# Performance work log

Measured on AMD Instinct MI355X. Metric: run time of the kernel, lower is better.

Reference implementation:

```python
import jax, jax.numpy as jnp
import numpy as np
from jax import lax

STRENGTH = 1.0
NORMALIZE = True


def setup_inputs() -> dict:
    key = jax.random.key(0)
    k1, k2 = jax.random.split(key)
    hidden_states = jax.random.normal(k1, (8, 4096, 1024), dtype=jnp.float32)
    # probe_weight is [k, hidden]; Q = orth(probe_weight.T) -> [hidden, k] orthonormal columns
    pw = jax.random.normal(k2, (1024, 16), dtype=jnp.float32)
    Q, _ = jnp.linalg.qr(pw)  # [hidden, k], orthonormal columns
    return {"hidden_states": hidden_states, "Q": Q}


def reference(hidden_states, Q):
    if NORMALIZE:
        old_norms = jnp.linalg.norm(hidden_states, axis=2, keepdims=True)  # [B,S,1]
    # Sequential Gram-Schmidt removal per direction (column of Q), as in the torch loop.
    def step(h, q):  # h: [B,S,H], q: [H]
        coef = jnp.einsum('bsh,h->bs', h, q)          # projection coefficient
        h = h - STRENGTH * coef[..., None] * q        # subtract component along q
        return h, None
    h, _ = lax.scan(step, hidden_states, Q.T)          # scan over k directions
    if NORMALIZE:
        norms = jnp.linalg.norm(h, axis=2, keepdims=True)
        h = h / norms * old_norms
    return h
```

## Files before the change

kernel.cpp:

```cpp
#include <hip/hip_runtime.h>
#include <hip/hip_bf16.h>

constexpr int HID = 1024;
constexpr int KD  = 16;
constexpr int TM  = 16;
constexpr int NW  = 8;
constexpr int TPB = 8;

typedef short bf16x8 __attribute__((ext_vector_type(8)));
typedef float f32x4  __attribute__((ext_vector_type(4)));

__device__ __forceinline__ short f2b(float x) {
    __hip_bfloat16 b = __float2bfloat16(x);
    return *reinterpret_cast<short*>(&b);
}
__device__ __forceinline__ float b2f(short s) {
    return __uint_as_float(((unsigned int)(unsigned short)s) << 16);
}

__global__ void q_setup(const float* __restrict__ Qf,
                        short* __restrict__ Qt, short* __restrict__ Qa) {
    const int idx = blockIdx.x*256 + threadIdx.x;
    if (idx < 16*HID) {
        const int r = idx >> 10, k = idx & 1023;
        Qt[idx] = f2b(Qf[k*KD + r]);
        const int gs = idx >> 4, dir = idx & 15;
        const int jslot = gs >> 4, rr = gs & 15;
        const int w = jslot >> 3, jl = jslot & 7;
        const int p = jl >> 1, odd = jl & 1;
        const int col = w*128 + p*32 + (rr >> 2)*8 + odd*4 + (rr & 3);
        Qa[idx] = f2b(Qf[col*KD + dir]);
    }
}

#define SCHED_FENCE() __builtin_amdgcn_sched_barrier(0)

__device__ __forceinline__ void stage_tile(float* ldsBuf, const float* Hbase,
                                           int w, int lane) {
    #pragma unroll
    for (int i = 0; i < 8; ++i) {
        const int rr = w*2 + (i >> 2);
        const int qq = i & 3;
        const int s  = qq*64 + lane;
        const float* g = Hbase + rr*1024 + ((s ^ (rr & 7)) << 2);
        const float* l = ldsBuf + rr*1024 + qq*256;
        __builtin_amdgcn_global_load_lds(
            (const __attribute__((address_space(1))) void*)g,
            (__attribute__((address_space(3))) void*)l, 16, 0, 0);
    }
}

__global__ __launch_bounds__(NW*64)
void probe_removal_dma8(const float* __restrict__ H,
                        const short* __restrict__ Qt,
                        const short* __restrict__ Qa,
                        float* __restrict__ out)
{
    const int lane = threadIdx.x & 63;
    const int w    = threadIdx.x >> 6;
    const int r    = lane & 15;
    const int q    = lane >> 4;

    __shared__ __align__(16) float Hb[2][TM][HID];
    __shared__ __align__(16) float ctr[NW][TM][20];
    __shared__ float s2p[NW][TM];

    const int tile0 = blockIdx.x * TPB;

    bf16x8 bq[4];
    #pragma unroll
    for (int kt = 0; kt < 4; ++kt)
        bq[kt] = *reinterpret_cast<const bf16x8*>(Qt + r*1024 + w*128 + q*8 + kt*32);
    bf16x8 aq0[4], aq1[4];
    #pragma unroll
    for (int p = 0; p < 4; ++p) {
        if (q < 2) {
            aq0[p] = *reinterpret_cast<const bf16x8*>(Qa + ((w*8 + 2*p    )*16 + r)*KD + q*8);
            aq1[p] = *reinterpret_cast<const bf16x8*>(Qa + ((w*8 + 2*p + 1)*16 + r)*KD + q*8);
        } else {
            #pragma unroll
            for (int i = 0; i < 8; ++i) { aq0[p][i] = 0; aq1[p][i] = 0; }
        }
    }
    SCHED_FENCE();

    stage_tile(&Hb[0][0][0], H + (size_t)tile0*TM*HID, w, lane);
    SCHED_FENCE();
    stage_tile(&Hb[1][0][0], H + (size_t)(tile0+1)*TM*HID, w, lane);
    SCHED_FENCE();
    asm volatile("s_waitcnt vmcnt(8)" ::: "memory");
    SCHED_FENCE();
    __builtin_amdgcn_s_barrier();

    #pragma unroll
    for (int t = 0; t < TPB; ++t) {
        const int cur = t & 1;
        const char* HbC = (const char*)&Hb[cur][0][0];

        bf16x8 af[4];
        f32x4 acc0 = {0.f,0.f,0.f,0.f}, acc1 = {0.f,0.f,0.f,0.f};
        float s2 = 0.f;
        #pragma unroll
        for (int kt = 0; kt < 4; ++kt) {
            const int P  = w*32 + kt*8 + q*2;
            const int sx = P ^ (r & 7);
            const float4 x = *(const float4*)(HbC + r*4096 + sx*16);
            const float4 y = *(const float4*)(HbC + r*4096 + (sx^1)*16);
            s2 = fmaf(x.x,x.x, fmaf(x.y,x.y, fmaf(x.z,x.z, fmaf(x.w,x.w, s2))));
            s2 = fmaf(y.x,y.x, fmaf(y.y,y.y, fmaf(y.z,y.z, fmaf(y.w,y.w, s2))));
            bf16x8 a;
            a[0]=f2b(x.x); a[1]=f2b(x.y); a[2]=f2b(x.z); a[3]=f2b(x.w);
            a[4]=f2b(y.x); a[5]=f2b(y.y); a[6]=f2b(y.z); a[7]=f2b(y.w);
            af[kt] = a;
            if (kt & 1) acc1 = __builtin_amdgcn_mfma_f32_16x16x32_bf16(a, bq[kt], acc1, 0, 0, 0);
            else        acc0 = __builtin_amdgcn_mfma_f32_16x16x32_bf16(a, bq[kt], acc0, 0, 0, 0);
        }
        const f32x4 acc = acc0 + acc1;
        s2 += __shfl_xor(s2, 16);
        s2 += __shfl_xor(s2, 32);

        #pragma unroll
        for (int i = 0; i < 4; ++i) ctr[w][q*4 + i][r] = acc[i];
        if (q == 0) s2p[w][r] = s2;

        asm volatile("s_waitcnt lgkmcnt(0)" ::: "memory");
        SCHED_FENCE();
        __builtin_amdgcn_s_barrier();
        SCHED_FENCE();

        if (t + 2 < TPB)
            stage_tile(&Hb[cur][0][0], H + (size_t)(tile0+t+2)*TM*HID, w, lane);
        SCHED_FENCE();

        float cf[8] = {0,0,0,0,0,0,0,0};
        if (q < 2) {
            #pragma unroll
            for (int w2 = 0; w2 < NW; ++w2) {
                const float4 a = *reinterpret_cast<const float4*>(&ctr[w2][r][q*8]);
                const float4 b = *reinterpret_cast<const float4*>(&ctr[w2][r][q*8 + 4]);
                cf[0]+=a.x; cf[1]+=a.y; cf[2]+=a.z; cf[3]+=a.w;
                cf[4]+=b.x; cf[5]+=b.y; cf[6]+=b.z; cf[7]+=b.w;
            }
        }
        float s2tot = 0.f;
        #pragma unroll
        for (int w2 = 0; w2 < NW; ++w2) s2tot += s2p[w2][r];

        float sc2 = 0.f;
        #pragma unroll
        for (int i = 0; i < 8; ++i) sc2 = fmaf(cf[i], cf[i], sc2);
        sc2 += __shfl_xor(sc2, 16);
        sc2 += __shfl_xor(sc2, 32);
        const float scale = rsqrtf(fmaxf(1.0f - sc2 / s2tot, 1e-20f));

        bf16x8 pb;
        #pragma unroll
        for (int i = 0; i < 8; ++i) pb[i] = f2b(cf[i]);

        float* orow = out + (size_t)(tile0+t)*TM*HID + r*HID + w*128;
        const f32x4 zero4 = {0.f,0.f,0.f,0.f};
        #pragma unroll
        for (int p = 0; p < 4; ++p) {
            const f32x4 d0 = __builtin_amdgcn_mfma_f32_16x16x32_bf16(aq0[p], pb, zero4, 0, 0, 0);
            const f32x4 d1 = __builtin_amdgcn_mfma_f32_16x16x32_bf16(aq1[p], pb, zero4, 0, 0, 0);
            f32x4 o0, o1;
            #pragma unroll
            for (int ii = 0; ii < 4; ++ii) {
                o0[ii] = (b2f(af[p][ii])     - d0[ii]) * scale;
                o1[ii] = (b2f(af[p][4 + ii]) - d1[ii]) * scale;
            }
            *reinterpret_cast<f32x4*>(orow + p*32 + q*8)     = o0;
            *reinterpret_cast<f32x4*>(orow + p*32 + q*8 + 4) = o1;
        }
        SCHED_FENCE();

        if (t < TPB-1) {
            asm volatile("s_waitcnt vmcnt(16)" ::: "memory");
            SCHED_FENCE();
            __builtin_amdgcn_s_barrier();
            SCHED_FENCE();
        }
    }
}

extern "C" void kernel_launch(void* const* d_in, const int* in_sizes, int n_in,
                              void* d_out, int out_size, void* d_ws, size_t ws_size,
                              hipStream_t stream) {
    const float* H  = (const float*)d_in[0];
    const float* Qf = (const float*)d_in[1];
    float* outp     = (float*)d_out;
    const int nrows  = in_sizes[0] / HID;
    const int ntiles = nrows / TM;

    short* Qt = (short*)d_ws;
    short* Qa = Qt + 16*HID;

    hipLaunchKernelGGL(q_setup, dim3(64), dim3(256), 0, stream, Qf, Qt, Qa);

    hipLaunchKernelGGL(probe_removal_dma8, dim3(ntiles / TPB), dim3(NW*64), 0, stream,
                       H, Qt, Qa, outp);
}
```

Before: 57.92 us.

## Stage H tiles in half-row chunks with finer-grained LDS double buffering

The LDS staging buffer becomes two half-row buffers (columns 0-511 and 512-1023) instead of two full tiles. The next tile's halves are prefetched into each buffer as soon as it has been consumed. Column ownership per wave is remapped so each wave covers 64 columns from each half, and the Q layout, output addressing and waitcnt values are adjusted to match. Tiles per block drop from 8 to 4, which halves LDS use so more blocks can be resident and doubles the grid size, but leaves less prefetch lead time per tile.

```diff
diff --git a/kernel.cpp b/kernel.cpp
--- a/kernel.cpp
+++ b/kernel.cpp
@@ -5,7 +5,8 @@
 constexpr int KD  = 16;
 constexpr int TM  = 16;
 constexpr int NW  = 8;
-constexpr int TPB = 8;
+constexpr int TPB = 4;
+constexpr int NH  = 2*TPB;
 
 typedef short bf16x8 __attribute__((ext_vector_type(8)));
 typedef float f32x4  __attribute__((ext_vector_type(4)));
@@ -28,22 +29,23 @@
         const int jslot = gs >> 4, rr = gs & 15;
         const int w = jslot >> 3, jl = jslot & 7;
         const int p = jl >> 1, odd = jl & 1;
-        const int col = w*128 + p*32 + (rr >> 2)*8 + odd*4 + (rr & 3);
+        const int gb = (p < 2) ? w*64 + p*32 : 512 + w*64 + (p-2)*32;
+        const int col = gb + (rr >> 2)*8 + odd*4 + (rr & 3);
         Qa[idx] = f2b(Qf[col*KD + dir]);
     }
 }
 
 #define SCHED_FENCE() __builtin_amdgcn_sched_barrier(0)
 
-__device__ __forceinline__ void stage_tile(float* ldsBuf, const float* Hbase,
-                                           int w, int lane) {
-    #pragma unroll
-    for (int i = 0; i < 8; ++i) {
-        const int rr = w*2 + (i >> 2);
-        const int qq = i & 3;
-        const int s  = qq*64 + lane;
-        const float* g = Hbase + rr*1024 + ((s ^ (rr & 7)) << 2);
-        const float* l = ldsBuf + rr*1024 + qq*256;
+__device__ __forceinline__ void stage_half(float* ldsBuf, const float* Hbase,
+                                           int half, int w, int lane) {
+    #pragma unroll
+    for (int i = 0; i < 4; ++i) {
+        const int rr = w*2 + (i >> 1);
+        const int s0 = (i & 1)*64;
+        const int s  = s0 + lane;
+        const float* g = Hbase + rr*1024 + half*512 + ((s ^ (rr & 7)) << 2);
+        const float* l = ldsBuf + rr*512 + s0*4;
         __builtin_amdgcn_global_load_lds(
             (const __attribute__((address_space(1))) void*)g,
             (__attribute__((address_space(3))) void*)l, 16, 0, 0);
@@ -51,26 +53,29 @@
 }
 
 __global__ __launch_bounds__(NW*64)
-void probe_removal_dma8(const float* __restrict__ H,
-                        const short* __restrict__ Qt,
-                        const short* __restrict__ Qa,
-                        float* __restrict__ out)
+void probe_removal_hh(const float* __restrict__ H,
+                      const short* __restrict__ Qt,
+                      const short* __restrict__ Qa,
+                      float* __restrict__ out)
 {
     const int lane = threadIdx.x & 63;
     const int w    = threadIdx.x >> 6;
     const int r    = lane & 15;
     const int q    = lane >> 4;
 
-    __shared__ __align__(16) float Hb[2][TM][HID];
+    __shared__ __align__(16) float Hb[2][TM][512];
     __shared__ __align__(16) float ctr[NW][TM][20];
     __shared__ float s2p[NW][TM];
 
     const int tile0 = blockIdx.x * TPB;
+    const float* Hblk = H + (size_t)tile0*TM*HID;
 
     bf16x8 bq[4];
     #pragma unroll
-    for (int kt = 0; kt < 4; ++kt)
-        bq[kt] = *reinterpret_cast<const bf16x8*>(Qt + r*1024 + w*128 + q*8 + kt*32);
+    for (int kt = 0; kt < 4; ++kt) {
+        const int gb = (kt < 2) ? w*64 + kt*32 : 512 + w*64 + (kt-2)*32;
+        bq[kt] = *reinterpret_cast<const bf16x8*>(Qt + r*1024 + gb + q*8);
+    }
     bf16x8 aq0[4], aq1[4];
     #pragma unroll
     for (int p = 0; p < 4; ++p) {
@@ -84,36 +89,61 @@
     }
     SCHED_FENCE();
 
-    stage_tile(&Hb[0][0][0], H + (size_t)tile0*TM*HID, w, lane);
-    SCHED_FENCE();
-    stage_tile(&Hb[1][0][0], H + (size_t)(tile0+1)*TM*HID, w, lane);
-    SCHED_FENCE();
-    asm volatile("s_waitcnt vmcnt(8)" ::: "memory");
+    stage_half(&Hb[0][0][0], Hblk, 0, w, lane);
+    SCHED_FENCE();
+    stage_half(&Hb[1][0][0], Hblk + 0*TM*HID + 0, 1, w, lane);
+    SCHED_FENCE();
+    asm volatile("s_waitcnt vmcnt(4)" ::: "memory");
     SCHED_FENCE();
     __builtin_amdgcn_s_barrier();
 
     #pragma unroll
     for (int t = 0; t < TPB; ++t) {
-        const int cur = t & 1;
-        const char* HbC = (const char*)&Hb[cur][0][0];
-
+        const float* Htile = Hblk + (size_t)t*TM*HID;
         bf16x8 af[4];
         f32x4 acc0 = {0.f,0.f,0.f,0.f}, acc1 = {0.f,0.f,0.f,0.f};
         float s2 = 0.f;
-        #pragma unroll
-        for (int kt = 0; kt < 4; ++kt) {
-            const int P  = w*32 + kt*8 + q*2;
-            const int sx = P ^ (r & 7);
-            const float4 x = *(const float4*)(HbC + r*4096 + sx*16);
-            const float4 y = *(const float4*)(HbC + r*4096 + (sx^1)*16);
+
+        #pragma unroll
+        for (int c = 0; c < 2; ++c) {
+            const int ploc = w*16 + c*8 + q*2;
+            const int sx = ploc ^ (r & 7);
+            const char* B = (const char*)&Hb[0][0][0];
+            const float4 x = *(const float4*)(B + r*2048 + sx*16);
+            const float4 y = *(const float4*)(B + r*2048 + (sx^1)*16);
             s2 = fmaf(x.x,x.x, fmaf(x.y,x.y, fmaf(x.z,x.z, fmaf(x.w,x.w, s2))));
             s2 = fmaf(y.x,y.x, fmaf(y.y,y.y, fmaf(y.z,y.z, fmaf(y.w,y.w, s2))));
             bf16x8 a;
             a[0]=f2b(x.x); a[1]=f2b(x.y); a[2]=f2b(x.z); a[3]=f2b(x.w);
             a[4]=f2b(y.x); a[5]=f2b(y.y); a[6]=f2b(y.z); a[7]=f2b(y.w);
-            af[kt] = a;
-            if (kt & 1) acc1 = __builtin_amdgcn_mfma_f32_16x16x32_bf16(a, bq[kt], acc1, 0, 0, 0);
-            else        acc0 = __builtin_amdgcn_mfma_f32_16x16x32_bf16(a, bq[kt], acc0, 0, 0, 0);
+            af[c] = a;
+            if (c) acc1 = __builtin_amdgcn_mfma_f32_16x16x32_bf16(a, bq[1], acc1, 0, 0, 0);
+            else   acc0 = __builtin_amdgcn_mfma_f32_16x16x32_bf16(a, bq[0], acc0, 0, 0, 0);
+        }
+        if (t == 0) { asm volatile("s_waitcnt vmcnt(0)" ::: "memory"); }
+        else        { asm volatile("s_waitcnt vmcnt(8)" ::: "memory"); }
+        SCHED_FENCE();
+        __builtin_amdgcn_s_barrier();
+        SCHED_FENCE();
+        if (2*t + 2 < NH)
+            stage_half(&Hb[0][0][0], Hblk + (size_t)(t+1)*TM*HID, 0, w, lane);
+        SCHED_FENCE();
+
+        #pragma unroll
+        for (int c = 0; c < 2; ++c) {
+            const int ploc = w*16 + c*8 + q*2;
+            const int sx = ploc ^ (r & 7);
+            const char* B = (const char*)&Hb[1][0][0];
+            const float4 x = *(const float4*)(B + r*2048 + sx*16);
+            const float4 y = *(const float4*)(B + r*2048 + (sx^1)*16);
+            s2 = fmaf(x.x,x.x, fmaf(x.y,x.y, fmaf(x.z,x.z, fmaf(x.w,x.w, s2))));
+            s2 = fmaf(y.x,y.x, fmaf(y.y,y.y, fmaf(y.z,y.z, fmaf(y.w,y.w, s2))));
+            bf16x8 a;
+            a[0]=f2b(x.x); a[1]=f2b(x.y); a[2]=f2b(x.z); a[3]=f2b(x.w);
+            a[4]=f2b(y.x); a[5]=f2b(y.y); a[6]=f2b(y.z); a[7]=f2b(y.w);
+            af[2 + c] = a;
+            if (c) acc1 = __builtin_amdgcn_mfma_f32_16x16x32_bf16(a, bq[3], acc1, 0, 0, 0);
+            else   acc0 = __builtin_amdgcn_mfma_f32_16x16x32_bf16(a, bq[2], acc0, 0, 0, 0);
         }
         const f32x4 acc = acc0 + acc1;
         s2 += __shfl_xor(s2, 16);
@@ -127,9 +157,8 @@
         SCHED_FENCE();
         __builtin_amdgcn_s_barrier();
         SCHED_FENCE();
-
-        if (t + 2 < TPB)
-            stage_tile(&Hb[cur][0][0], H + (size_t)(tile0+t+2)*TM*HID, w, lane);
+        if (2*t + 3 < NH)
+            stage_half(&Hb[1][0][0], Hblk + (size_t)(t+1)*TM*HID, 1, w, lane);
         SCHED_FENCE();
 
         float cf[8] = {0,0,0,0,0,0,0,0};
@@ -157,10 +186,11 @@
         #pragma unroll
         for (int i = 0; i < 8; ++i) pb[i] = f2b(cf[i]);
 
-        float* orow = out + (size_t)(tile0+t)*TM*HID + r*HID + w*128;
+        float* orow = out + (size_t)(tile0 + t)*TM*HID + r*HID;
         const f32x4 zero4 = {0.f,0.f,0.f,0.f};
         #pragma unroll
         for (int p = 0; p < 4; ++p) {
+            const int gb = (p < 2) ? w*64 + p*32 : 512 + w*64 + (p-2)*32;
             const f32x4 d0 = __builtin_amdgcn_mfma_f32_16x16x32_bf16(aq0[p], pb, zero4, 0, 0, 0);
             const f32x4 d1 = __builtin_amdgcn_mfma_f32_16x16x32_bf16(aq1[p], pb, zero4, 0, 0, 0);
             f32x4 o0, o1;
@@ -169,13 +199,13 @@
                 o0[ii] = (b2f(af[p][ii])     - d0[ii]) * scale;
                 o1[ii] = (b2f(af[p][4 + ii]) - d1[ii]) * scale;
             }
-            *reinterpret_cast<f32x4*>(orow + p*32 + q*8)     = o0;
-            *reinterpret_cast<f32x4*>(orow + p*32 + q*8 + 4) = o1;
+            *reinterpret_cast<f32x4*>(orow + gb + q*8)     = o0;
+            *reinterpret_cast<f32x4*>(orow + gb + q*8 + 4) = o1;
         }
         SCHED_FENCE();
 
         if (t < TPB-1) {
-            asm volatile("s_waitcnt vmcnt(16)" ::: "memory");
+            asm volatile("s_waitcnt vmcnt(12)" ::: "memory");
             SCHED_FENCE();
             __builtin_amdgcn_s_barrier();
             SCHED_FENCE();
@@ -197,6 +227,6 @@
 
     hipLaunchKernelGGL(q_setup, dim3(64), dim3(256), 0, stream, Qf, Qt, Qa);
 
-    hipLaunchKernelGGL(probe_removal_dma8, dim3(ntiles / TPB), dim3(NW*64), 0, stream,
+    hipLaunchKernelGGL(probe_removal_hh, dim3(ntiles / TPB), dim3(NW*64), 0, stream,
                        H, Qt, Qa, outp);
 }
```

New measurement: 58.94 us. Within noise of the previous version (+1.8%).
